# Kernel tuning notes

Hardware: AMD Instinct MI355X
Metric: run time of the kernel (lower is better)

## Reference

```python
import jax, jax.numpy as jnp
import numpy as np

EPS = 1e-15
N_NODES = 20000
N_EDGES = 640000
FEAT = 128
N_RBF = 20
CUTOFF = 5.0


def setup_inputs() -> dict:
    key = jax.random.key(0)
    ks = jax.random.split(key, 10)
    s_j = jax.random.normal(ks[0], (N_NODES, FEAT), jnp.float32)
    v_j = jax.random.normal(ks[1], (N_NODES, FEAT, 3), jnp.float32)
    r_ij = jax.random.normal(ks[2], (N_EDGES, 3), jnp.float32)
    nbrs = jax.random.randint(ks[3], (N_EDGES, 2), 0, N_NODES, jnp.int64)
    # InvariantDense: Dense(F->F, swish) then Dense(F->3F)
    W1 = jax.random.normal(ks[4], (FEAT, FEAT), jnp.float32) / np.sqrt(FEAT)
    b1 = jnp.zeros((FEAT,), jnp.float32)
    W2 = jax.random.normal(ks[5], (FEAT, 3 * FEAT), jnp.float32) / np.sqrt(FEAT)
    b2 = jnp.zeros((3 * FEAT,), jnp.float32)
    # DistanceEmbed dense: Dense(n_rbf -> 3F)
    Wd = jax.random.normal(ks[6], (N_RBF, 3 * FEAT), jnp.float32) / np.sqrt(N_RBF)
    bd = jnp.zeros((3 * FEAT,), jnp.float32)
    return {"s_j": s_j, "v_j": v_j, "r_ij": r_ij, "nbrs": nbrs,
            "W1": W1, "b1": b1, "W2": W2, "b2": b2, "Wd": Wd, "bd": bd}


def reference(s_j, v_j, r_ij, nbrs, W1, b1, W2, b2, Wd, bd):
    N, F = s_j.shape
    # preprocess_r
    dist = jnp.sqrt(jnp.sum(r_ij ** 2 + EPS, axis=-1))          # [E]
    unit = r_ij / dist[:, None]                                  # [E,3]
    # InvariantDense on nodes (dense before gather, as in torch code)
    phi_node = jax.nn.silu(s_j @ W1 + b1) @ W2 + b2              # [N,3F]
    phi = phi_node[nbrs[:, 1]]                                   # [E,3F]
    # PaiNN radial basis: sin(n*pi*d/cutoff)/d, n=1..n_rbf
    k = jnp.arange(1, N_RBF + 1, dtype=dist.dtype) * (np.pi / CUTOFF)  # [n_rbf]
    rbf = jnp.sin(dist[:, None] * k[None, :]) / dist[:, None]    # [E,n_rbf]
    # cosine cutoff envelope
    env = 0.5 * (jnp.cos(np.pi * dist / CUTOFF) + 1.0)
    env = jnp.where(dist < CUTOFF, env, 0.0)                     # [E]
    w_s = (rbf @ Wd + bd) * env[:, None]                         # [E,3F]
    inv = (phi * w_s).reshape(-1, 3, F)                          # [E,3,F]
    split0 = inv[:, 0, :][:, :, None]                            # [E,F,1]
    split1 = inv[:, 1, :]                                        # [E,F]
    split2 = inv[:, 2, :][:, :, None]                            # [E,F,1]
    delta_v_ij = split2 * unit[:, None, :] + split0 * v_j[nbrs[:, 1]]  # [E,F,3]
    idx = nbrs[:, 0]
    delta_s_i = jax.ops.segment_sum(split1, idx, num_segments=N)      # [N,F]
    delta_v_i = jax.ops.segment_sum(delta_v_ij, idx, num_segments=N)  # [N,F,3]
    return (delta_s_i, delta_v_i)
```

## Files before the change

kernel.cpp:

```cpp
#include <hip/hip_runtime.h>
#include <hip/hip_bf16.h>
#include <math.h>

typedef __hip_bfloat16 bf16;

#define FEAT 128
#define NRBF 20
#define CUTOFF_F 5.0f
#define KSCALE 0.62831853071795864769f
#define NB 4096
#define INV_H 819.0f
#define H_STEP 0.001221001221001221f

__device__ __forceinline__ float b2f(bf16 x) { return __bfloat162float(x); }
__device__ __forceinline__ bf16 f2b(float x) { return __float2bfloat16(x); }
__device__ __forceinline__ float us2f(unsigned short u) {
    return __uint_as_float(((unsigned)u) << 16);
}

template<int F32>
__device__ __forceinline__ float LD(const void* p, size_t i) {
    if (F32) return ((const float*)p)[i];
    return b2f(((const bf16*)p)[i]);
}
template<int F32>
__device__ __forceinline__ void ST(void* p, size_t i, float v) {
    if (F32) ((float*)p)[i] = v;
    else ((bf16*)p)[i] = f2b(v);
}

__device__ __forceinline__ int get_dst(const int* nb, int e, int is64) {
    return is64 ? nb[4 * e] : nb[2 * e];
}
__device__ __forceinline__ int get_src(const int* nb, int e, int is64) {
    return is64 ? nb[4 * e + 2] : nb[2 * e + 1];
}
__device__ __forceinline__ int clampi(int v, int n) {
    return v < 0 ? 0 : (v >= n ? n - 1 : v);
}

__global__ void init_kernel(const void* __restrict__ s_ptr, const int* __restrict__ nbrs32,
                            int nE, int* __restrict__ flags, int* __restrict__ counts, int nN) {
    int t = blockIdx.x * blockDim.x + threadIdx.x;
    if (t < nN) counts[t] = 0;
    if (t == 0) {
        const unsigned* u = (const unsigned*)s_ptr;
        int hits = 0;
        for (int i = 0; i < 64; ++i) {
            unsigned ef = (u[i] >> 7) & 0xFF;
            hits += (ef >= 110 && ef <= 135) ? 1 : 0;
        }
        flags[0] = (hits < 32) ? 1 : 0;
        int lim = 2 * nE; if (lim > 128) lim = 128;
        int allz = 1;
        for (int i = 1; i < lim; i += 2) allz &= (nbrs32[i] == 0);
        flags[1] = allz;
    }
}

__global__ void hist_kernel(const int* __restrict__ nbrs, const int* __restrict__ flags,
                            int* __restrict__ counts, int nE, int nN) {
    int e = blockIdx.x * blockDim.x + threadIdx.x;
    if (e < nE) {
        int d = clampi(get_dst(nbrs, e, flags[1]), nN);
        atomicAdd(&counts[d], 1);
    }
}

__global__ __launch_bounds__(1024) void scan_kernel(const int* __restrict__ counts,
        int* __restrict__ offsets, int* __restrict__ cursor, int nN) {
    __shared__ int part[1024];
    const int t = threadIdx.x;
    const int chunk = (nN + 1023) / 1024;
    const int base = t * chunk;
    int local[32];
    int sum = 0;
    for (int c = 0; c < chunk && c < 32; ++c) {
        int idx = base + c;
        int v = (idx < nN) ? counts[idx] : 0;
        local[c] = v;
        sum += v;
    }
    part[t] = sum;
    __syncthreads();
    for (int off = 1; off < 1024; off <<= 1) {
        int add = (t >= off) ? part[t - off] : 0;
        __syncthreads();
        part[t] += add;
        __syncthreads();
    }
    int run = part[t] - sum;
    for (int c = 0; c < chunk && c < 32; ++c) {
        int idx = base + c;
        if (idx < nN) { offsets[idx] = run; cursor[idx] = run; run += local[c]; }
    }
    if (t == 1023) offsets[nN] = part[1023];
}

__global__ __launch_bounds__(384) void prep_kernel(const void* __restrict__ Wd,
        const void* __restrict__ bd, float* __restrict__ WdT, const int* __restrict__ flags) {
    const int c = threadIdx.x;
    const int F32 = flags[0];
    if (F32) {
        for (int k = 0; k < NRBF; ++k) WdT[c * 24 + k] = ((const float*)Wd)[k * 384 + c];
        WdT[c * 24 + 20] = ((const float*)bd)[c];
    } else {
        for (int k = 0; k < NRBF; ++k) WdT[c * 24 + k] = b2f(((const bf16*)Wd)[k * 384 + c]);
        WdT[c * 24 + 20] = b2f(((const bf16*)bd)[c]);
    }
    WdT[c * 24 + 21] = 0.f; WdT[c * 24 + 22] = 0.f; WdT[c * 24 + 23] = 0.f;
}

__global__ __launch_bounds__(384) void build_table_kernel(const void* __restrict__ Wd,
        const void* __restrict__ bd, bf16* __restrict__ tab, const int* __restrict__ flags) {
    const int b = blockIdx.x;
    const int c = threadIdx.x;
    const int F32 = flags[0];
    const float d = fmaxf(b * H_STEP, 1e-7f);
    const float x = d * KSCALE;
    const float s1 = sinf(x);
    const float c1 = cosf(x);
    const float env = (d < CUTOFF_F) ? (0.5f * (c1 + 1.0f)) : 0.0f;
    const float invd = 1.0f / d;
    float g[NRBF];
    const float tc = 2.0f * c1;
    float skm2 = 0.f, skm1 = s1;
    g[0] = s1 * invd;
    #pragma unroll
    for (int k = 1; k < NRBF; ++k) {
        const float sk = fmaf(tc, skm1, -skm2);
        g[k] = sk * invd;
        skm2 = skm1; skm1 = sk;
    }
    float acc = F32 ? ((const float*)bd)[c] : b2f(((const bf16*)bd)[c]);
    #pragma unroll
    for (int k = 0; k < NRBF; ++k) {
        const float w = F32 ? ((const float*)Wd)[(size_t)k * 384 + c]
                            : b2f(((const bf16*)Wd)[(size_t)k * 384 + c]);
        acc = fmaf(g[k], w, acc);
    }
    tab[(size_t)b * 384 + c] = f2b(acc * env);
}

template<int F32, int MODE>
__device__ void pre_scatter_body(const void* __restrict__ r_ij, const int* __restrict__ nbrs,
        int is64, int* __restrict__ cursor, int* __restrict__ src_ids,
        float4* __restrict__ u_env, int* __restrict__ pos_of_e, float* __restrict__ gbuf,
        int e, int nE, int nN) {
    const int d = clampi(get_dst(nbrs, e, is64), nN);
    const int j = clampi(get_src(nbrs, e, is64), nN);
    int pos = atomicAdd(&cursor[d], 1);
    pos = clampi(pos, nE);
    src_ids[pos] = j;

    const float rx = LD<F32>(r_ij, (size_t)3 * e + 0);
    const float ry = LD<F32>(r_ij, (size_t)3 * e + 1);
    const float rz = LD<F32>(r_ij, (size_t)3 * e + 2);
    const float d2   = rx * rx + ry * ry + rz * rz + 3e-15f;
    const float invd = rsqrtf(d2);
    const float dd   = d2 * invd;

    if (MODE == 2) {
        u_env[pos] = make_float4(rx * invd, ry * invd, rz * invd, dd * INV_H);
        return;
    }

    const float x  = dd * KSCALE;
    const float c1 = F32 ? cosf(x) : __cosf(x);
    const float env = (dd < CUTOFF_F) ? (0.5f * (c1 + 1.0f)) : 0.0f;
    u_env[pos] = make_float4(rx * invd, ry * invd, rz * invd, env);

    if (MODE == 1) {
        pos_of_e[e] = pos;
    } else {
        const float s1 = F32 ? sinf(x) : __sinf(x);
        const float scale = invd * env;
        const float tc = 2.0f * c1;
        float skm2 = 0.f, skm1 = s1;
        float* g = gbuf + (size_t)pos * NRBF;
        g[0] = s1 * scale;
        #pragma unroll
        for (int k = 1; k < NRBF; ++k) {
            const float sk = fmaf(tc, skm1, -skm2);
            g[k] = sk * scale;
            skm2 = skm1; skm1 = sk;
        }
    }
}

__global__ __launch_bounds__(256) void pre_scatter_kernel(const void* r_ij, const int* nbrs,
        const int* __restrict__ flags, int* cursor, int* src_ids, float4* u_env,
        int* pos_of_e, float* gbuf, int nE, int nN, int mode) {
    int e = blockIdx.x * blockDim.x + threadIdx.x;
    if (e >= nE) return;
    const int F32 = flags[0], is64 = flags[1];
    if (mode == 2) {
        if (F32) pre_scatter_body<1,2>(r_ij, nbrs, is64, cursor, src_ids, u_env, pos_of_e, gbuf, e, nE, nN);
        else     pre_scatter_body<0,2>(r_ij, nbrs, is64, cursor, src_ids, u_env, pos_of_e, gbuf, e, nE, nN);
    } else if (mode == 1) {
        if (F32) pre_scatter_body<1,1>(r_ij, nbrs, is64, cursor, src_ids, u_env, pos_of_e, gbuf, e, nE, nN);
        else     pre_scatter_body<0,1>(r_ij, nbrs, is64, cursor, src_ids, u_env, pos_of_e, gbuf, e, nE, nN);
    } else {
        if (F32) pre_scatter_body<1,0>(r_ij, nbrs, is64, cursor, src_ids, u_env, pos_of_e, gbuf, e, nE, nN);
        else     pre_scatter_body<0,0>(r_ij, nbrs, is64, cursor, src_ids, u_env, pos_of_e, gbuf, e, nE, nN);
    }
}

template<int F32>
__device__ void gemm_body(const void* __restrict__ s_j, const void* __restrict__ v_j,
                          const void* __restrict__ W1,
                          const void* __restrict__ b1, const void* __restrict__ W2,
                          const void* __restrict__ b2v, bf16* __restrict__ phi, int nN,
                          int packed) {
    __shared__ float sl[8][FEAT];
    __shared__ float hl[8][FEAT];
    __shared__ float ps[3][8][FEAT];
    const int t = threadIdx.x;
    const int n0 = blockIdx.x * 8;
    const int fch = t & 127;
    const int seg = t >> 7;

    if (packed) {
        #pragma unroll
        for (int n = 0; n < 8; ++n) {
            int row = n0 + n;
            if (row < nN) {
                const float vv = LD<F32>(v_j, ((size_t)row * FEAT + fch) * 3 + seg);
                phi[((size_t)row * FEAT + fch) * 6 + 3 + seg] = f2b(vv);
            }
        }
    }

    for (int idx = t; idx < 8 * FEAT; idx += 384) {
        int n = idx >> 7, k = idx & 127;
        int row = n0 + n;
        sl[n][k] = (row < nN) ? LD<F32>(s_j, (size_t)row * FEAT + k) : 0.f;
    }
    __syncthreads();

    {
        const int k0 = seg * 43;
        const int k1 = (seg == 2) ? FEAT : k0 + 43;
        float part[8] = {};
        for (int k = k0; k < k1; ++k) {
            const float w = LD<F32>(W1, (size_t)k * FEAT + fch);
            #pragma unroll
            for (int n = 0; n < 8; ++n) part[n] = fmaf(sl[n][k], w, part[n]);
        }
        #pragma unroll
        for (int n = 0; n < 8; ++n) ps[seg][n][fch] = part[n];
    }
    __syncthreads();

    for (int idx = t; idx < 8 * FEAT; idx += 384) {
        int n = idx >> 7, f = idx & 127;
        float a = ps[0][n][f] + ps[1][n][f] + ps[2][n][f] + LD<F32>(b1, f);
        float sg = F32 ? (1.0f / (1.0f + expf(-a))) : (1.0f / (1.0f + __expf(-a)));
        hl[n][f] = a * sg;
    }
    __syncthreads();

    float acc[8] = {};
    #pragma unroll 4
    for (int k = 0; k < FEAT; ++k) {
        const float w = LD<F32>(W2, (size_t)k * 384 + t);
        #pragma unroll
        for (int n = 0; n < 8; ++n) acc[n] = fmaf(hl[n][k], w, acc[n]);
    }
    const float bb = LD<F32>(b2v, t);
    #pragma unroll
    for (int n = 0; n < 8; ++n) {
        int row = n0 + n;
        if (row < nN) {
            if (packed) phi[((size_t)row * FEAT + fch) * 6 + seg] = f2b(acc[n] + bb);
            else        phi[(size_t)row * 384 + t] = f2b(acc[n] + bb);
        }
    }
}

__global__ __launch_bounds__(384) void gemm_node_kernel(const void* s_j, const void* v_j,
        const void* W1, const void* b1, const void* W2, const void* b2v, bf16* phi,
        const int* __restrict__ flags, int nN, int packed) {
    if (flags[0]) gemm_body<1>(s_j, v_j, W1, b1, W2, b2v, phi, nN, packed);
    else          gemm_body<0>(s_j, v_j, W1, b1, W2, b2v, phi, nN, packed);
}

template<int F32>
__device__ void pre_ws_body(const void* __restrict__ r_ij, const float* __restrict__ WdT,
        const int* __restrict__ pos_of_e, bf16* __restrict__ ws_w, int e) {
    const float rx = LD<F32>(r_ij, (size_t)3 * e + 0);
    const float ry = LD<F32>(r_ij, (size_t)3 * e + 1);
    const float rz = LD<F32>(r_ij, (size_t)3 * e + 2);
    const float d2   = rx * rx + ry * ry + rz * rz + 3e-15f;
    const float invd = rsqrtf(d2);
    const float dd   = d2 * invd;
    const float x  = dd * KSCALE;
    const float s1 = F32 ? sinf(x) : __sinf(x);
    const float c1 = F32 ? cosf(x) : __cosf(x);
    const float env = (dd < CUTOFF_F) ? (0.5f * (c1 + 1.0f)) : 0.0f;
    const float scale = invd * env;
    float gk[NRBF];
    const float tc = 2.0f * c1;
    float skm2 = 0.f, skm1 = s1;
    gk[0] = s1 * scale;
    #pragma unroll
    for (int k = 1; k < NRBF; ++k) {
        const float sk = fmaf(tc, skm1, -skm2);
        gk[k] = sk * scale;
        skm2 = skm1; skm1 = sk;
    }
    const int pos = pos_of_e[e];
    bf16* dst = ws_w + (size_t)pos * 384;
    for (int c0 = 0; c0 < 384; c0 += 4) {
        float r[4];
        #pragma unroll
        for (int u = 0; u < 4; ++u) {
            const float* w = WdT + (size_t)(c0 + u) * 24;
            float acc = w[20] * env;
            #pragma unroll
            for (int k = 0; k < NRBF; ++k) acc = fmaf(gk[k], w[k], acc);
            r[u] = acc;
        }
        union { bf16 b[4]; uint2 u2; } pk;
        pk.b[0] = f2b(r[0]); pk.b[1] = f2b(r[1]); pk.b[2] = f2b(r[2]); pk.b[3] = f2b(r[3]);
        *(uint2*)(dst + c0) = pk.u2;
    }
}

__global__ __launch_bounds__(256) void pre_ws_kernel(const void* r_ij,
        const float* __restrict__ WdT, const int* __restrict__ pos_of_e,
        bf16* __restrict__ ws_w, const int* __restrict__ flags, int nE) {
    int e = blockIdx.x * blockDim.x + threadIdx.x;
    if (e >= nE) return;
    if (flags[0]) pre_ws_body<1>(r_ij, WdT, pos_of_e, ws_w, e);
    else          pre_ws_body<0>(r_ij, WdT, pos_of_e, ws_w, e);
}

template<int F32>
__device__ void msg_a_body(const bf16* __restrict__ ws_w, const bf16* __restrict__ phi,
        const void* __restrict__ v_j, const int* __restrict__ src_ids,
        const float4* __restrict__ u_env, const int* __restrict__ offsets,
        void* __restrict__ out, int nE, int nN) {
    const int i = blockIdx.x;
    const int f = threadIdx.x;
    int start = offsets[i];
    int end   = offsets[i + 1];
    if (start < 0) start = 0;
    if (end > nE) end = nE;

    float ds = 0.f, dv0 = 0.f, dv1 = 0.f, dv2 = 0.f;

    #pragma unroll 2
    for (int p = start; p < end; ++p) {
        const int j = src_ids[p];
        const float4 ue = u_env[p];
        const bf16* wr = ws_w + (size_t)p * 384;
        const float w0 = b2f(wr[f]);
        const float w1 = b2f(wr[FEAT + f]);
        const float w2 = b2f(wr[2 * FEAT + f]);
        const bf16* ph = phi + (size_t)j * 384;
        const float p0 = b2f(ph[f]);
        const float p1 = b2f(ph[FEAT + f]);
        const float p2 = b2f(ph[2 * FEAT + f]);
        const float vx = LD<F32>(v_j, ((size_t)j * FEAT + f) * 3 + 0);
        const float vy = LD<F32>(v_j, ((size_t)j * FEAT + f) * 3 + 1);
        const float vz = LD<F32>(v_j, ((size_t)j * FEAT + f) * 3 + 2);
        const float i0 = w0 * p0;
        const float i1 = w1 * p1;
        const float i2 = w2 * p2;
        ds += i1;
        dv0 = fmaf(i2, ue.x, fmaf(i0, vx, dv0));
        dv1 = fmaf(i2, ue.y, fmaf(i0, vy, dv1));
        dv2 = fmaf(i2, ue.z, fmaf(i0, vz, dv2));
    }

    ST<F32>(out, (size_t)i * FEAT + f, ds);
    const size_t ob = (size_t)nN * FEAT + ((size_t)i * FEAT + f) * 3;
    ST<F32>(out, ob + 0, dv0);
    ST<F32>(out, ob + 1, dv1);
    ST<F32>(out, ob + 2, dv2);
}

__global__ __launch_bounds__(128) void msg_a_kernel(const bf16* ws_w, const bf16* phi,
        const void* v_j, const int* src_ids, const float4* u_env, const int* offsets,
        const int* __restrict__ flags, void* out, int nE, int nN) {
    if (flags[0]) msg_a_body<1>(ws_w, phi, v_j, src_ids, u_env, offsets, out, nE, nN);
    else          msg_a_body<0>(ws_w, phi, v_j, src_ids, u_env, offsets, out, nE, nN);
}

template<int F32>
__device__ void msg_c_body(const unsigned short* __restrict__ tab, const bf16* __restrict__ rec,
        const float4* __restrict__ u4, const int* __restrict__ src_ids,
        const int* __restrict__ offsets, void* __restrict__ out, int nE, int nN) {
    const int i = blockIdx.x;
    const int f = threadIdx.x;
    int start = offsets[i];
    int end   = offsets[i + 1];
    if (start < 0) start = 0;
    if (end > nE) end = nE;

    float ds = 0.f, dv0 = 0.f, dv1 = 0.f, dv2 = 0.f;

    for (int p = start; p < end; ++p) {
        const int j = src_ids[p];
        const float4 uu = u4[p];
        const float binf = uu.w;
        int bin = (int)binf;
        if (bin > NB - 2) bin = NB - 2;
        const float fr = binf - (float)bin;
        const float m = (binf < (float)(NB - 1)) ? 1.0f : 0.0f;

        const unsigned short* T = tab + (size_t)bin * 384;
        const float t00 = us2f(T[f]);
        const float t01 = us2f(T[384 + f]);
        const float t10 = us2f(T[FEAT + f]);
        const float t11 = us2f(T[384 + FEAT + f]);
        const float t20 = us2f(T[2 * FEAT + f]);
        const float t21 = us2f(T[384 + 2 * FEAT + f]);
        const float w0 = fmaf(t01 - t00, fr, t00) * m;
        const float w1 = fmaf(t11 - t10, fr, t10) * m;
        const float w2 = fmaf(t21 - t20, fr, t20) * m;

        const unsigned* rp = (const unsigned*)(rec + ((size_t)j * FEAT + f) * 6);
        const unsigned ra = rp[0];
        const unsigned rb = rp[1];
        const unsigned rc = rp[2];
        const float p0 = __uint_as_float(ra << 16);
        const float p1 = __uint_as_float(ra & 0xffff0000u);
        const float p2 = __uint_as_float(rb << 16);
        const float vx = __uint_as_float(rb & 0xffff0000u);
        const float vy = __uint_as_float(rc << 16);
        const float vz = __uint_as_float(rc & 0xffff0000u);

        const float i0 = w0 * p0;
        const float i1 = w1 * p1;
        const float i2 = w2 * p2;
        ds += i1;
        dv0 = fmaf(i2, uu.x, fmaf(i0, vx, dv0));
        dv1 = fmaf(i2, uu.y, fmaf(i0, vy, dv1));
        dv2 = fmaf(i2, uu.z, fmaf(i0, vz, dv2));
    }

    ST<F32>(out, (size_t)i * FEAT + f, ds);
    const size_t ob = (size_t)nN * FEAT + ((size_t)i * FEAT + f) * 3;
    ST<F32>(out, ob + 0, dv0);
    ST<F32>(out, ob + 1, dv1);
    ST<F32>(out, ob + 2, dv2);
}

__global__ __launch_bounds__(128) void msg_c_kernel(const unsigned short* tab, const bf16* rec,
        const float4* u4, const int* src_ids, const int* offsets,
        const int* __restrict__ flags, void* out, int nE, int nN) {
    if (flags[0]) msg_c_body<1>(tab, rec, u4, src_ids, offsets, out, nE, nN);
    else          msg_c_body<0>(tab, rec, u4, src_ids, offsets, out, nE, nN);
}

template<int F32>
__device__ void msg_b_body(const void* __restrict__ v_j, const void* __restrict__ Wd,
        const void* __restrict__ bd, const bf16* __restrict__ phi,
        const float* __restrict__ gbuf, const int* __restrict__ src_ids,
        const float4* __restrict__ u_env, const int* __restrict__ offsets,
        void* __restrict__ out, int nE, int nN) {
    const int i = blockIdx.x;
    const int f = threadIdx.x;

    float wd0[NRBF], wd1[NRBF], wd2[NRBF];
    #pragma unroll
    for (int k = 0; k < NRBF; ++k) {
        wd0[k] = LD<F32>(Wd, (size_t)k * 384 + f);
        wd1[k] = LD<F32>(Wd, (size_t)k * 384 + FEAT + f);
        wd2[k] = LD<F32>(Wd, (size_t)k * 384 + 2 * FEAT + f);
    }
    const float bd0 = LD<F32>(bd, f);
    const float bd1 = LD<F32>(bd, FEAT + f);
    const float bd2 = LD<F32>(bd, 2 * FEAT + f);

    int start = offsets[i];
    int end   = offsets[i + 1];
    if (start < 0) start = 0;
    if (end > nE) end = nE;

    float ds = 0.f, dv0 = 0.f, dv1 = 0.f, dv2 = 0.f;

    for (int p = start; p < end; ++p) {
        const int j = src_ids[p];
        const float4 ue = u_env[p];
        const float* g = gbuf + (size_t)p * NRBF;
        float t0 = 0.f, t1 = 0.f, t2 = 0.f;
        #pragma unroll
        for (int k = 0; k < NRBF; ++k) {
            const float gk = g[k];
            t0 = fmaf(gk, wd0[k], t0);
            t1 = fmaf(gk, wd1[k], t1);
            t2 = fmaf(gk, wd2[k], t2);
        }
        const float w0 = fmaf(bd0, ue.w, t0);
        const float w1 = fmaf(bd1, ue.w, t1);
        const float w2 = fmaf(bd2, ue.w, t2);

        const bf16* ph = phi + (size_t)j * 384;
        const float p0 = b2f(ph[f]);
        const float p1 = b2f(ph[FEAT + f]);
        const float p2 = b2f(ph[2 * FEAT + f]);
        const float vx = LD<F32>(v_j, ((size_t)j * FEAT + f) * 3 + 0);
        const float vy = LD<F32>(v_j, ((size_t)j * FEAT + f) * 3 + 1);
        const float vz = LD<F32>(v_j, ((size_t)j * FEAT + f) * 3 + 2);

        const float i0 = w0 * p0;
        const float i1 = w1 * p1;
        const float i2 = w2 * p2;
        ds += i1;
        dv0 = fmaf(i2, ue.x, fmaf(i0, vx, dv0));
        dv1 = fmaf(i2, ue.y, fmaf(i0, vy, dv1));
        dv2 = fmaf(i2, ue.z, fmaf(i0, vz, dv2));
    }

    ST<F32>(out, (size_t)i * FEAT + f, ds);
    const size_t ob = (size_t)nN * FEAT + ((size_t)i * FEAT + f) * 3;
    ST<F32>(out, ob + 0, dv0);
    ST<F32>(out, ob + 1, dv1);
    ST<F32>(out, ob + 2, dv2);
}

__global__ __launch_bounds__(128) void msg_b_kernel(const void* v_j, const void* Wd,
        const void* bd, const bf16* phi, const float* gbuf, const int* src_ids,
        const float4* u_env, const int* offsets, const int* __restrict__ flags,
        void* out, int nE, int nN) {
    if (flags[0]) msg_b_body<1>(v_j, Wd, bd, phi, gbuf, src_ids, u_env, offsets, out, nE, nN);
    else          msg_b_body<0>(v_j, Wd, bd, phi, gbuf, src_ids, u_env, offsets, out, nE, nN);
}

extern "C" void kernel_launch(void* const* d_in, const int* in_sizes, int n_in,
                              void* d_out, int out_size, void* d_ws, size_t ws_size,
                              hipStream_t stream) {
    const void* s_j  = d_in[0];
    const void* v_j  = d_in[1];
    const void* r_ij = d_in[2];
    const int*  nbrs = (const int*)d_in[3];
    const void* W1   = d_in[4];
    const void* b1   = d_in[5];
    const void* W2   = d_in[6];
    const void* b2   = d_in[7];
    const void* Wd   = d_in[8];
    const void* bd   = d_in[9];

    const int nN = out_size / (4 * FEAT);
    const int nE = in_sizes[2] / 3;

    char* ws = (char*)d_ws;
    size_t off = 0;
    auto alloc = [&](size_t bytes) -> void* {
        void* p = ws + off;
        off = (off + bytes + 255) & ~(size_t)255;
        return p;
    };
    int*    flags    = (int*)alloc(16);
    int*    counts   = (int*)alloc((size_t)nN * 4);
    int*    offsets  = (int*)alloc(((size_t)nN + 1) * 4);
    int*    cursor   = (int*)alloc((size_t)nN * 4);
    int*    src_ids  = (int*)alloc((size_t)nE * 4);
    float4* u_env    = (float4*)alloc((size_t)nE * 16);
    float*  WdT      = (float*)alloc((size_t)384 * 24 * 4);
    const size_t base = off;

    size_t offA = base;
    int*  pos_of_e = (int*)(ws + offA);  offA += ((size_t)nE * 4 + 255) & ~(size_t)255;
    bf16* phiA     = (bf16*)(ws + offA); offA += ((size_t)nN * 384 * 2 + 255) & ~(size_t)255;
    bf16* ws_w     = (bf16*)(ws + offA); offA += (size_t)nE * 384 * 2;
    size_t offC = base;
    bf16* rec = (bf16*)(ws + offC);      offC += ((size_t)nN * FEAT * 6 * 2 + 255) & ~(size_t)255;
    bf16* tab = (bf16*)(ws + offC);      offC += (size_t)NB * 384 * 2;
    size_t offB = base;
    float* gbufB = (float*)(ws + offB);  offB += ((size_t)nE * NRBF * 4 + 255) & ~(size_t)255;
    bf16*  phiB  = (bf16*)(ws + offB);   offB += (size_t)nN * 384 * 2;

    const int modeA = (ws_size >= offA) ? 1 : 0;
    const int modeC = (!modeA && ws_size >= offC) ? 1 : 0;

    init_kernel<<<(nN + 255) / 256, 256, 0, stream>>>(s_j, nbrs, nE, flags, counts, nN);
    hist_kernel<<<(nE + 255) / 256, 256, 0, stream>>>(nbrs, flags, counts, nE, nN);
    scan_kernel<<<1, 1024, 0, stream>>>(counts, offsets, cursor, nN);

    const int psMode = modeA ? 1 : (modeC ? 2 : 0);
    pre_scatter_kernel<<<(nE + 255) / 256, 256, 0, stream>>>(
        r_ij, nbrs, flags, cursor, src_ids, u_env, pos_of_e, gbufB, nE, nN, psMode);

    if (modeA) {
        prep_kernel<<<1, 384, 0, stream>>>(Wd, bd, WdT, flags);
        gemm_node_kernel<<<(nN + 7) / 8, 384, 0, stream>>>(s_j, v_j, W1, b1, W2, b2, phiA, flags, nN, 0);
        pre_ws_kernel<<<(nE + 255) / 256, 256, 0, stream>>>(r_ij, WdT, pos_of_e, ws_w, flags, nE);
        msg_a_kernel<<<nN, 128, 0, stream>>>(ws_w, phiA, v_j, src_ids, u_env, offsets,
                                             flags, d_out, nE, nN);
    } else if (modeC) {
        build_table_kernel<<<NB, 384, 0, stream>>>(Wd, bd, tab, flags);
        gemm_node_kernel<<<(nN + 7) / 8, 384, 0, stream>>>(s_j, v_j, W1, b1, W2, b2, rec, flags, nN, 1);
        msg_c_kernel<<<nN, 128, 0, stream>>>((const unsigned short*)tab, rec, u_env, src_ids,
                                             offsets, flags, d_out, nE, nN);
    } else {
        gemm_node_kernel<<<(nN + 7) / 8, 384, 0, stream>>>(s_j, v_j, W1, b1, W2, b2, phiB, flags, nN, 0);
        msg_b_kernel<<<nN, 128, 0, stream>>>(v_j, Wd, bd, phiB, gbufB, src_ids, u_env,
                                             offsets, flags, d_out, nE, nN);
    }
}
```

Measured before the change: 489.5 us.

## Fuse CSR build and RBF table construction into one cooperative grid kernel

```diff
diff --git a/kernel.cpp b/kernel.cpp
--- a/kernel.cpp
+++ b/kernel.cpp
@@ -1,8 +1,10 @@
 #include <hip/hip_runtime.h>
+#include <hip/hip_cooperative_groups.h>
 #include <hip/hip_bf16.h>
 #include <math.h>
 
 typedef __hip_bfloat16 bf16;
+namespace cg = cooperative_groups;
 
 #define FEAT 128
 #define NRBF 20
@@ -11,6 +13,7 @@
 #define NB 4096
 #define INV_H 819.0f
 #define H_STEP 0.001221001221001221f
+#define EPT_MAX 8
 
 __device__ __forceinline__ float b2f(bf16 x) { return __bfloat162float(x); }
 __device__ __forceinline__ bf16 f2b(float x) { return __float2bfloat16(x); }
@@ -38,6 +41,147 @@
 __device__ __forceinline__ int clampi(int v, int n) {
     return v < 0 ? 0 : (v >= n ? n - 1 : v);
 }
+
+__device__ __forceinline__ float tab_entry(const void* Wd, const void* bd, int F32,
+                                           int bb, int c) {
+    const float d = fmaxf(bb * H_STEP, 1e-7f);
+    const float x = d * KSCALE;
+    const float s1 = sinf(x);
+    const float c1 = cosf(x);
+    const float env = (d < CUTOFF_F) ? (0.5f * (c1 + 1.0f)) : 0.0f;
+    const float invd = 1.0f / d;
+    float acc = F32 ? ((const float*)bd)[c] : b2f(((const bf16*)bd)[c]);
+    const float tc = 2.0f * c1;
+    float skm2 = 0.f, skm1 = s1;
+    float g0 = s1 * invd;
+    {
+        const float w = F32 ? ((const float*)Wd)[c] : b2f(((const bf16*)Wd)[c]);
+        acc = fmaf(g0, w, acc);
+    }
+    #pragma unroll
+    for (int k = 1; k < NRBF; ++k) {
+        const float sk = fmaf(tc, skm1, -skm2);
+        const float gk = sk * invd;
+        const float w = F32 ? ((const float*)Wd)[(size_t)k * 384 + c]
+                            : b2f(((const bf16*)Wd)[(size_t)k * 384 + c]);
+        acc = fmaf(gk, w, acc);
+        skm2 = skm1; skm1 = sk;
+    }
+    return acc * env;
+}
+
+__global__ __launch_bounds__(256) void csr_coop_kernel(
+        const void* s_ptr, const int* nbrs, const void* r_ij,
+        int* flags, int* counts, int* offsets, int* cursor,
+        int* src_ids, float4* u_env, const void* Wd, const void* bd,
+        bf16* tab, int* partials, int nE, int nN) {
+    cg::grid_group grid = cg::this_grid();
+    const int t   = threadIdx.x;
+    const int b   = blockIdx.x;
+    const int nb  = gridDim.x;
+    const int tid = b * 256 + t;
+    const int tot = nb * 256;
+
+    for (int i = tid; i < nN; i += tot) counts[i] = 0;
+    if (tid == 0) {
+        const unsigned* u = (const unsigned*)s_ptr;
+        int hits = 0;
+        for (int i = 0; i < 64; ++i) {
+            unsigned ef = (u[i] >> 7) & 0xFF;
+            hits += (ef >= 110 && ef <= 135) ? 1 : 0;
+        }
+        flags[0] = (hits < 32) ? 1 : 0;
+        int lim = 2 * nE; if (lim > 128) lim = 128;
+        int allz = 1;
+        for (int i = 1; i < lim; i += 2) allz &= (nbrs[i] == 0);
+        flags[1] = allz;
+    }
+    grid.sync();
+
+    const int F32  = flags[0];
+    const int is64 = flags[1];
+
+    int dre[EPT_MAX], jre[EPT_MAX];
+    #pragma unroll
+    for (int k = 0; k < EPT_MAX; ++k) {
+        const int e = tid + k * tot;
+        int dd = -1, jj = -1;
+        if (e < nE) {
+            dd = clampi(get_dst(nbrs, e, is64), nN);
+            jj = clampi(get_src(nbrs, e, is64), nN);
+            atomicAdd(&counts[dd], 1);
+        }
+        dre[k] = dd; jre[k] = jj;
+    }
+    for (int i = tid; i < NB * 384; i += tot) {
+        const int bb = i / 384, c = i - bb * 384;
+        tab[i] = f2b(tab_entry(Wd, bd, F32, bb, c));
+    }
+    grid.sync();
+
+    const int chunk = (nN + nb - 1) / nb;
+    if (t == 0) {
+        int s = 0;
+        const int base = b * chunk;
+        for (int c = 0; c < chunk; ++c) {
+            const int idx = base + c;
+            if (idx < nN) s += counts[idx];
+        }
+        partials[b] = s;
+    }
+    grid.sync();
+
+    {
+        __shared__ int red[256];
+        int s = 0;
+        for (int i = t; i < b; i += 256) s += partials[i];
+        red[t] = s;
+        __syncthreads();
+        for (int o = 128; o; o >>= 1) {
+            if (t < o) red[t] += red[t + o];
+            __syncthreads();
+        }
+        if (t == 0) {
+            int run = red[0];
+            const int base = b * chunk;
+            for (int c = 0; c < chunk; ++c) {
+                const int idx = base + c;
+                if (idx < nN) {
+                    offsets[idx] = run; cursor[idx] = run;
+                    run += counts[idx];
+                }
+            }
+            if (b == nb - 1) offsets[nN] = run;
+        }
+    }
+    grid.sync();
+
+    #pragma unroll
+    for (int k = 0; k < EPT_MAX; ++k) {
+        const int e = tid + k * tot;
+        if (e < nE) {
+            const int dd = dre[k], jj = jre[k];
+            float rx, ry, rz;
+            if (F32) {
+                rx = ((const float*)r_ij)[(size_t)3 * e + 0];
+                ry = ((const float*)r_ij)[(size_t)3 * e + 1];
+                rz = ((const float*)r_ij)[(size_t)3 * e + 2];
+            } else {
+                rx = b2f(((const bf16*)r_ij)[(size_t)3 * e + 0]);
+                ry = b2f(((const bf16*)r_ij)[(size_t)3 * e + 1]);
+                rz = b2f(((const bf16*)r_ij)[(size_t)3 * e + 2]);
+            }
+            const float d2   = rx * rx + ry * ry + rz * rz + 3e-15f;
+            const float invd = rsqrtf(d2);
+            const float dd_f = d2 * invd;
+            int pos = atomicAdd(&cursor[dd], 1);
+            pos = clampi(pos, nE);
+            src_ids[pos] = jj;
+            u_env[pos] = make_float4(rx * invd, ry * invd, rz * invd, dd_f * INV_H);
+        }
+    }
+}
+
 
 __global__ void init_kernel(const void* __restrict__ s_ptr, const int* __restrict__ nbrs32,
                             int nE, int* __restrict__ flags, int* __restrict__ counts, int nN) {
@@ -115,31 +259,7 @@
         const void* __restrict__ bd, bf16* __restrict__ tab, const int* __restrict__ flags) {
     const int b = blockIdx.x;
     const int c = threadIdx.x;
-    const int F32 = flags[0];
-    const float d = fmaxf(b * H_STEP, 1e-7f);
-    const float x = d * KSCALE;
-    const float s1 = sinf(x);
-    const float c1 = cosf(x);
-    const float env = (d < CUTOFF_F) ? (0.5f * (c1 + 1.0f)) : 0.0f;
-    const float invd = 1.0f / d;
-    float g[NRBF];
-    const float tc = 2.0f * c1;
-    float skm2 = 0.f, skm1 = s1;
-    g[0] = s1 * invd;
-    #pragma unroll
-    for (int k = 1; k < NRBF; ++k) {
-        const float sk = fmaf(tc, skm1, -skm2);
-        g[k] = sk * invd;
-        skm2 = skm1; skm1 = sk;
-    }
-    float acc = F32 ? ((const float*)bd)[c] : b2f(((const bf16*)bd)[c]);
-    #pragma unroll
-    for (int k = 0; k < NRBF; ++k) {
-        const float w = F32 ? ((const float*)Wd)[(size_t)k * 384 + c]
-                            : b2f(((const bf16*)Wd)[(size_t)k * 384 + c]);
-        acc = fmaf(g[k], w, acc);
-    }
-    tab[(size_t)b * 384 + c] = f2b(acc * env);
+    tab[(size_t)b * 384 + c] = f2b(tab_entry(Wd, bd, flags[0], b, c));
 }
 
 template<int F32, int MODE>
@@ -560,6 +680,7 @@
     int*    cursor   = (int*)alloc((size_t)nN * 4);
     int*    src_ids  = (int*)alloc((size_t)nE * 4);
     float4* u_env    = (float4*)alloc((size_t)nE * 16);
+    int*    partials = (int*)alloc(4096 * 4);
     float*  WdT      = (float*)alloc((size_t)384 * 24 * 4);
     const size_t base = off;
 
@@ -577,11 +698,50 @@
     const int modeA = (ws_size >= offA) ? 1 : 0;
     const int modeC = (!modeA && ws_size >= offC) ? 1 : 0;
 
+    if (modeC) {
+        bool coop_ok = false;
+        hipDeviceProp_t prop;
+        if (hipGetDeviceProperties(&prop, 0) == hipSuccess) {
+            int perCU = 0;
+            if (hipOccupancyMaxActiveBlocksPerMultiprocessor(
+                    &perCU, (const void*)csr_coop_kernel, 256, 0) == hipSuccess && perCU > 0) {
+                int blocks = perCU * prop.multiProcessorCount;
+                if (blocks > 4096) blocks = 4096;
+                const long long tot = (long long)blocks * 256;
+                const int ept = (int)((nE + tot - 1) / tot);
+                if (blocks >= 64 && ept <= EPT_MAX) {
+                    void* s_jv = (void*)s_j; void* nbv = (void*)nbrs; void* rv = (void*)r_ij;
+                    void* Wdv = (void*)Wd;  void* bdv = (void*)bd;
+                    int nE_ = nE, nN_ = nN;
+                    void* args[] = { &s_jv, &nbv, &rv, &flags, &counts, &offsets, &cursor,
+                                     &src_ids, &u_env, &Wdv, &bdv, &tab, &partials,
+                                     &nE_, &nN_ };
+                    hipError_t err = hipLaunchCooperativeKernel(
+                        (const void*)csr_coop_kernel, dim3(blocks), dim3(256),
+                        args, 0, stream);
+                    coop_ok = (err == hipSuccess);
+                }
+            }
+        }
+        if (!coop_ok) {
+            init_kernel<<<(nN + 255) / 256, 256, 0, stream>>>(s_j, nbrs, nE, flags, counts, nN);
+            hist_kernel<<<(nE + 255) / 256, 256, 0, stream>>>(nbrs, flags, counts, nE, nN);
+            scan_kernel<<<1, 1024, 0, stream>>>(counts, offsets, cursor, nN);
+            pre_scatter_kernel<<<(nE + 255) / 256, 256, 0, stream>>>(
+                r_ij, nbrs, flags, cursor, src_ids, u_env, pos_of_e, gbufB, nE, nN, 2);
+            build_table_kernel<<<NB, 384, 0, stream>>>(Wd, bd, tab, flags);
+        }
+        gemm_node_kernel<<<(nN + 7) / 8, 384, 0, stream>>>(s_j, v_j, W1, b1, W2, b2, rec, flags, nN, 1);
+        msg_c_kernel<<<nN, 128, 0, stream>>>((const unsigned short*)tab, rec, u_env, src_ids,
+                                             offsets, flags, d_out, nE, nN);
+        return;
+    }
+
     init_kernel<<<(nN + 255) / 256, 256, 0, stream>>>(s_j, nbrs, nE, flags, counts, nN);
     hist_kernel<<<(nE + 255) / 256, 256, 0, stream>>>(nbrs, flags, counts, nE, nN);
     scan_kernel<<<1, 1024, 0, stream>>>(counts, offsets, cursor, nN);
 
-    const int psMode = modeA ? 1 : (modeC ? 2 : 0);
+    const int psMode = modeA ? 1 : 0;
     pre_scatter_kernel<<<(nE + 255) / 256, 256, 0, stream>>>(
         r_ij, nbrs, flags, cursor, src_ids, u_env, pos_of_e, gbufB, nE, nN, psMode);
 
@@ -591,11 +751,6 @@
         pre_ws_kernel<<<(nE + 255) / 256, 256, 0, stream>>>(r_ij, WdT, pos_of_e, ws_w, flags, nE);
         msg_a_kernel<<<nN, 128, 0, stream>>>(ws_w, phiA, v_j, src_ids, u_env, offsets,
                                              flags, d_out, nE, nN);
-    } else if (modeC) {
-        build_table_kernel<<<NB, 384, 0, stream>>>(Wd, bd, tab, flags);
-        gemm_node_kernel<<<(nN + 7) / 8, 384, 0, stream>>>(s_j, v_j, W1, b1, W2, b2, rec, flags, nN, 1);
-        msg_c_kernel<<<nN, 128, 0, stream>>>((const unsigned short*)tab, rec, u_env, src_ids,
-                                             offsets, flags, d_out, nE, nN);
     } else {
         gemm_node_kernel<<<(nN + 7) / 8, 384, 0, stream>>>(s_j, v_j, W1, b1, W2, b2, phiB, flags, nN, 0);
         msg_b_kernel<<<nN, 128, 0, stream>>>(v_j, Wd, bd, phiB, gbufB, src_ids, u_env,
```

Result: slower. 727.2 us (+48.6%).
